# Kernel tuning notes

Measured on AMD Instinct MI355X. Metric: run time of the kernel, lower is better.

Reference implementation:

```python
import jax, jax.numpy as jnp
import numpy as np

B, D, C = 8192, 256, 128
MARGIN = 0.5
REPULSION_WEIGHT = 1.0
ALPHA = 0.5
BETA = 0.5
EPS = 1e-6  # F.pairwise_distance default eps, added to the difference vector


def make_centers(num_classes=C, embedding_dim=D):
    # center[k] is +/-1 one-hot along axis (k % embedding_dim)
    idx = np.arange(num_classes)
    centers = np.zeros((num_classes, embedding_dim), dtype=np.float32)
    centers[idx, idx % embedding_dim] = np.where(idx % 2 == 0, 1.0, -1.0)
    return jnp.asarray(centers)


def setup_inputs() -> dict:
    key = jax.random.key(0)
    k1, k2, k3 = jax.random.split(key, 3)
    features = jax.random.normal(k1, (B, D), dtype=jnp.float32)
    classification = jax.random.normal(k2, (B, C), dtype=jnp.float32)
    labels = jax.random.randint(k3, (B,), 0, C, dtype=jnp.int32)
    return {"features": features, "classification": classification, "labels": labels}


def _sculpted_loss(embeddings, labels, centers):
    b = embeddings.shape[0]
    # attractive: MSE to per-sample class center, mean over all elements
    center_targets = centers[labels]  # [B, D]
    attractive = jnp.mean((embeddings - center_targets) ** 2)

    # repulsive: for pairs i<j with different labels,
    # relu(margin - ||e_i - e_j + eps||_2)^2, summed then / (B(B-1)/2).
    sq_norm = jnp.sum(embeddings ** 2, axis=1)          # [B]
    row_sum = jnp.sum(embeddings, axis=1)               # [B]
    gram = embeddings @ embeddings.T                    # [B, B]
    sq = (sq_norm[:, None] + sq_norm[None, :] - 2.0 * gram
          + 2.0 * EPS * (row_sum[:, None] - row_sum[None, :])
          + embeddings.shape[1] * (EPS * EPS))
    dist = jnp.sqrt(jnp.maximum(sq, 1e-12))             # [B, B]

    iu = jnp.triu(jnp.ones((b, b), dtype=bool), k=1)    # i < j
    diff_label = labels[:, None] != labels[None, :]
    mask = iu & diff_label
    hinge = jnp.maximum(MARGIN - dist, 0.0)
    repulsive = jnp.sum(jnp.where(mask, hinge * hinge, 0.0))
    repulsive = repulsive / (b * (b - 1) / 2.0)

    return attractive + REPULSION_WEIGHT * repulsive


def reference(features, classification, labels):
    centers = make_centers()
    # cross entropy (mean over batch)
    logp = jax.nn.log_softmax(classification, axis=-1)
    ce = -jnp.mean(jnp.take_along_axis(logp, labels[:, None].astype(jnp.int32), axis=1)[:, 0])
    contrastive = _sculpted_loss(features, labels, centers)
    return BETA * contrastive + ALPHA * ce
```

## Files before the change

kernel.cpp:

```cpp
#include <hip/hip_runtime.h>
#include <stdint.h>

#define B_N   8192
#define D_DIM 256
#define C_CLS 128
#define EPSV  1e-6f
#define DEPS  (256.0f * EPSV * EPSV)
#define NT    64
#define NTRI  (NT * (NT + 1) / 2)
#define PLANE (B_N * 16)

typedef float f32x4 __attribute__((ext_vector_type(4)));
typedef long long llx2 __attribute__((ext_vector_type(2)));

__device__ __forceinline__ unsigned f2fp8(float v) {
    unsigned u = __float_as_uint(v);
    unsigned s = (u >> 24) & 0x80;
    unsigned a = u & 0x7fffffff;
    if (a > 0x43E00000u) a = 0x43E00000u;
    a += 0x7FFFF + ((a >> 20) & 1);
    int e = (int)(a >> 23) - 120;
    if (e <= 0) return s;
    return s | ((unsigned)e << 3) | ((a >> 20) & 7);
}


__global__ __launch_bounds__(256) void k_prep(
        const float* __restrict__ feat, const float* __restrict__ cls,
        const int* __restrict__ labels, unsigned char* __restrict__ e8,
        float* __restrict__ aR, float* __restrict__ bC,
        float* __restrict__ attrP, float* __restrict__ ceP) {
    int t = threadIdx.x, lane = t & 63, w = t >> 6;
    int row = blockIdx.x * 4 + w;
    int lab = labels[row];

    const float4* src = (const float4*)(feat + (size_t)row * D_DIM);
    float4 f = src[lane];
    unsigned pk = f2fp8(f.x) | (f2fp8(f.y) << 8) | (f2fp8(f.z) << 16) | (f2fp8(f.w) << 24);
    {
        int plane = ((lane >> 4) << 2) | ((lane >> 1) & 3);
        int off   = (((lane >> 3) & 1) << 3) | ((lane & 1) << 2);
        *(unsigned*)(e8 + (size_t)plane * PLANE + row * 16 + off) = pk;
    }

    float sq = f.x*f.x + f.y*f.y + f.z*f.z + f.w*f.w;
    float sm = f.x + f.y + f.z + f.w;
    float arr[4] = {f.x, f.y, f.z, f.w};
    float pick = ((lab >> 2) == lane) ? arr[lab & 3] : 0.f;

    const float2* csrc = (const float2*)(cls + (size_t)row * C_CLS);
    float2 c2 = csrc[lane];
    float mx = fmaxf(c2.x, c2.y);
    #pragma unroll
    for (int off = 32; off; off >>= 1) mx = fmaxf(mx, __shfl_xor(mx, off));
    float es = expf(c2.x - mx) + expf(c2.y - mx);
    float cpick = ((lab >> 1) == lane) ? ((lab & 1) ? c2.y : c2.x) : 0.f;

    #pragma unroll
    for (int off = 32; off; off >>= 1) {
        sq    += __shfl_xor(sq, off);
        sm    += __shfl_xor(sm, off);
        pick  += __shfl_xor(pick, off);
        es    += __shfl_xor(es, off);
        cpick += __shfl_xor(cpick, off);
    }
    __shared__ float wsumA[4], wsumC[4];
    if (lane == 0) {
        aR[row] = sq + 2.f * EPSV * sm;
        bC[row] = sq - 2.f * EPSV * sm + DEPS;
        float s = (lab & 1) ? -1.f : 1.f;
        wsumA[w] = sq - 2.f * s * pick + 1.f;
        wsumC[w] = -(cpick - mx - logf(es));
    }
    __syncthreads();
    if (t == 0) {
        attrP[blockIdx.x] = wsumA[0] + wsumA[1] + wsumA[2] + wsumA[3];
        ceP[blockIdx.x]   = wsumC[0] + wsumC[1] + wsumC[2] + wsumC[3];
    }
}

__global__ __launch_bounds__(256, 3) void k_gram(
        const unsigned char* __restrict__ e8, const float* __restrict__ aR,
        const float* __restrict__ bC, const int* __restrict__ labels,
        float* __restrict__ repP) {
    int t = threadIdx.x, lane = t & 63, w = t >> 6;

    int swz = (blockIdx.x & 7) * (NTRI / 8) + (blockIdx.x >> 3);

    int bid = swz, tm = 0;
    while (bid >= NT - tm) { bid -= NT - tm; tm++; }
    int tn = tm + bid;

    int l15 = lane & 15, quad = lane >> 4;
    int wr = w >> 1, wc = w & 1;
    int m0 = tm * 128 + wr * 64, n0 = tn * 128 + wc * 64;

    unsigned rowA[4], rowB[4];
    #pragma unroll
    for (int i = 0; i < 4; i++) {
        rowA[i] = (unsigned)(m0 + i * 16 + l15) * 16;
        rowB[i] = (unsigned)(n0 + i * 16 + l15) * 16;
    }

    f32x4 acc[4][4] = {};
    llx2 avA[4], bvA[4], avB[4], bvB[4];
    float am[16], bn[4];

    {
        const unsigned char* b0 = e8 + (size_t)quad * PLANE;
        #pragma unroll
        for (int mi = 0; mi < 4; mi++) avA[mi] = *(const llx2*)(b0 + rowA[mi]);
        #pragma unroll
        for (int ni = 0; ni < 4; ni++) bvA[ni] = *(const llx2*)(b0 + rowB[ni]);
    }

    #pragma unroll
    for (int tp = 0; tp < 4; tp++) {
        llx2* ca = (tp & 1) ? avB : avA;
        llx2* cb = (tp & 1) ? bvB : bvA;
        llx2* na = (tp & 1) ? avA : avB;
        llx2* nb = (tp & 1) ? bvA : bvB;
        if (tp < 3) {
            const unsigned char* bnx = e8 + (size_t)(4 * (tp + 1) + quad) * PLANE;
            #pragma unroll
            for (int mi = 0; mi < 4; mi++) na[mi] = *(const llx2*)(bnx + rowA[mi]);
            #pragma unroll
            for (int ni = 0; ni < 4; ni++) nb[ni] = *(const llx2*)(bnx + rowB[ni]);
        } else {
            #pragma unroll
            for (int ni = 0; ni < 4; ni++) bn[ni] = bC[n0 + ni * 16 + l15];
            #pragma unroll
            for (int mi = 0; mi < 4; mi++)
                #pragma unroll
                for (int r = 0; r < 4; r++)
                    am[mi * 4 + r] = aR[m0 + mi * 16 + quad * 4 + r];
        }
        __builtin_amdgcn_s_setprio(1);
        #pragma unroll
        for (int p = 0; p < 2; p++)
            #pragma unroll
            for (int mi = 0; mi < 4; mi++)
                #pragma unroll
                for (int ni = 0; ni < 4; ni++)
                    acc[mi][ni] = __builtin_amdgcn_mfma_f32_16x16x32_fp8_fp8(
                        ca[mi][p], cb[ni][p], acc[mi][ni], 0, 0, 0);
        __builtin_amdgcn_s_setprio(0);
    }

    float minv = 1e30f;
    #pragma unroll
    for (int mi = 0; mi < 4; mi++)
        #pragma unroll
        for (int ni = 0; ni < 4; ni++)
            #pragma unroll
            for (int r = 0; r < 4; r++)
                minv = fminf(minv, fmaf(-2.f, acc[mi][ni][r], am[mi * 4 + r] + bn[ni]));
    #pragma unroll
    for (int off = 32; off; off >>= 1) minv = fminf(minv, __shfl_xor(minv, off));

    float rep = 0.f;
    if (minv < 0.25f) {
        int ln[4];
        #pragma unroll
        for (int ni = 0; ni < 4; ni++) ln[ni] = labels[n0 + ni * 16 + l15];
        #pragma unroll
        for (int mi = 0; mi < 4; mi++) {
            #pragma unroll
            for (int r = 0; r < 4; r++) {
                int m = m0 + mi * 16 + quad * 4 + r;
                int lm = labels[m];
                #pragma unroll
                for (int ni = 0; ni < 4; ni++) {
                    int n = n0 + ni * 16 + l15;
                    float sq   = fmaf(-2.f, acc[mi][ni][r], am[mi * 4 + r] + bn[ni]);
                    float dist = sqrtf(fmaxf(sq, 1e-12f));
                    float h    = fmaxf(0.5f - dist, 0.f);
                    rep += (lm != ln[ni] && m < n) ? h * h : 0.f;
                }
            }
        }
        #pragma unroll
        for (int off = 32; off; off >>= 1) rep += __shfl_xor(rep, off);
    }
    if (lane == 0) repP[swz * 4 + w] = rep;
}

__global__ __launch_bounds__(256) void k_final(
        const float* __restrict__ P, float* __restrict__ out) {
    int t = threadIdx.x, lane = t & 63, w = t >> 6;
    const float4* P4 = (const float4*)P;
    float a = 0.f, c = 0.f, r = 0.f;
    for (int i = t; i < 512; i += 256) {
        float4 va = P4[i], vc = P4[512 + i];
        a += va.x + va.y + va.z + va.w;
        c += vc.x + vc.y + vc.z + vc.w;
    }
    for (int i = t; i < 2080; i += 256) {
        float4 vr = P4[1024 + i];
        r += vr.x + vr.y + vr.z + vr.w;
    }
    #pragma unroll
    for (int off = 32; off; off >>= 1) {
        a += __shfl_xor(a, off);
        c += __shfl_xor(c, off);
        r += __shfl_xor(r, off);
    }
    __shared__ float sa[4], sc[4], sr[4];
    if (lane == 0) { sa[w] = a; sc[w] = c; sr[w] = r; }
    __syncthreads();
    if (t == 0) {
        float attr = (sa[0] + sa[1] + sa[2] + sa[3]) / (float)((size_t)B_N * D_DIM);
        float ce   = (sc[0] + sc[1] + sc[2] + sc[3]) / (float)B_N;
        float rep  = (sr[0] + sr[1] + sr[2] + sr[3]) / ((float)B_N * (float)(B_N - 1) * 0.5f);
        out[0] = 0.5f * (attr + rep) + 0.5f * ce;
    }
}

extern "C" void kernel_launch(void* const* d_in, const int* in_sizes, int n_in,
                              void* d_out, int out_size, void* d_ws, size_t ws_size,
                              hipStream_t stream) {
    const float* feat   = (const float*)d_in[0];
    const float* cls    = (const float*)d_in[1];
    const int*   labels = (const int*)d_in[2];
    float* out = (float*)d_out;

    float*          P    = (float*)d_ws;
    unsigned char*  e8   = (unsigned char*)d_ws + 65536;
    float*          aR   = (float*)((char*)d_ws + 65536 + (size_t)B_N * D_DIM);
    float*          bC   = aR + B_N;

    k_prep <<<2048, 256, 0, stream>>>(feat, cls, labels, e8, aR, bC, P, P + 2048);
    k_gram <<<NTRI, 256, 0, stream>>>(e8, aR, bC, labels, P + 4096);
    k_final<<<1, 256, 0, stream>>>(P, out);
}
```

Baseline: 91.91 us.

## Prune gram tiles early using partial-dimension distance lower bound

The gram kernel now accumulates only the first 64 feature dimensions and computes a per-row norm and sum over that slice in the prep kernel. That gives a lower bound on each pairwise squared distance. If every pair in a tile has a partial squared distance at or above a safe threshold, the tile writes zero and exits without loading or multiplying the remaining three quarters of the data. The cost is extra prep outputs, the loss of double-buffered prefetching on the full path, and a data-dependent branch. Tiles near the diagonal or with close pairs still pay the full cost.

```diff
diff --git a/kernel.cpp b/kernel.cpp
--- a/kernel.cpp
+++ b/kernel.cpp
@@ -6,6 +6,7 @@
 #define C_CLS 128
 #define EPSV  1e-6f
 #define DEPS  (256.0f * EPSV * EPSV)
+#define D64EPS (64.0f * EPSV * EPSV)
 #define NT    64
 #define NTRI  (NT * (NT + 1) / 2)
 #define PLANE (B_N * 16)
@@ -29,6 +30,7 @@
         const float* __restrict__ feat, const float* __restrict__ cls,
         const int* __restrict__ labels, unsigned char* __restrict__ e8,
         float* __restrict__ aR, float* __restrict__ bC,
+        float* __restrict__ aR64, float* __restrict__ bC64,
         float* __restrict__ attrP, float* __restrict__ ceP) {
     int t = threadIdx.x, lane = t & 63, w = t >> 6;
     int row = blockIdx.x * 4 + w;
@@ -45,6 +47,8 @@
 
     float sq = f.x*f.x + f.y*f.y + f.z*f.z + f.w*f.w;
     float sm = f.x + f.y + f.z + f.w;
+    float sq64 = (lane < 16) ? sq : 0.f;
+    float sm64 = (lane < 16) ? sm : 0.f;
     float arr[4] = {f.x, f.y, f.z, f.w};
     float pick = ((lab >> 2) == lane) ? arr[lab & 3] : 0.f;
 
@@ -60,14 +64,18 @@
     for (int off = 32; off; off >>= 1) {
         sq    += __shfl_xor(sq, off);
         sm    += __shfl_xor(sm, off);
+        sq64  += __shfl_xor(sq64, off);
+        sm64  += __shfl_xor(sm64, off);
         pick  += __shfl_xor(pick, off);
         es    += __shfl_xor(es, off);
         cpick += __shfl_xor(cpick, off);
     }
     __shared__ float wsumA[4], wsumC[4];
     if (lane == 0) {
-        aR[row] = sq + 2.f * EPSV * sm;
-        bC[row] = sq - 2.f * EPSV * sm + DEPS;
+        aR[row]   = sq + 2.f * EPSV * sm;
+        bC[row]   = sq - 2.f * EPSV * sm + DEPS;
+        aR64[row] = sq64 + 2.f * EPSV * sm64;
+        bC64[row] = sq64 - 2.f * EPSV * sm64 + D64EPS;
         float s = (lab & 1) ? -1.f : 1.f;
         wsumA[w] = sq - 2.f * s * pick + 1.f;
         wsumC[w] = -(cpick - mx - logf(es));
@@ -81,7 +89,8 @@
 
 __global__ __launch_bounds__(256, 3) void k_gram(
         const unsigned char* __restrict__ e8, const float* __restrict__ aR,
-        const float* __restrict__ bC, const int* __restrict__ labels,
+        const float* __restrict__ bC, const float* __restrict__ aR64,
+        const float* __restrict__ bC64, const int* __restrict__ labels,
         float* __restrict__ repP) {
     int t = threadIdx.x, lane = t & 63, w = t >> 6;
 
@@ -103,38 +112,58 @@
     }
 
     f32x4 acc[4][4] = {};
-    llx2 avA[4], bvA[4], avB[4], bvB[4];
-    float am[16], bn[4];
+    llx2 av[4], bv[4];
 
     {
         const unsigned char* b0 = e8 + (size_t)quad * PLANE;
         #pragma unroll
-        for (int mi = 0; mi < 4; mi++) avA[mi] = *(const llx2*)(b0 + rowA[mi]);
-        #pragma unroll
-        for (int ni = 0; ni < 4; ni++) bvA[ni] = *(const llx2*)(b0 + rowB[ni]);
-    }
-
-    #pragma unroll
-    for (int tp = 0; tp < 4; tp++) {
-        llx2* ca = (tp & 1) ? avB : avA;
-        llx2* cb = (tp & 1) ? bvB : bvA;
-        llx2* na = (tp & 1) ? avA : avB;
-        llx2* nb = (tp & 1) ? bvA : bvB;
-        if (tp < 3) {
-            const unsigned char* bnx = e8 + (size_t)(4 * (tp + 1) + quad) * PLANE;
-            #pragma unroll
-            for (int mi = 0; mi < 4; mi++) na[mi] = *(const llx2*)(bnx + rowA[mi]);
-            #pragma unroll
-            for (int ni = 0; ni < 4; ni++) nb[ni] = *(const llx2*)(bnx + rowB[ni]);
-        } else {
-            #pragma unroll
-            for (int ni = 0; ni < 4; ni++) bn[ni] = bC[n0 + ni * 16 + l15];
-            #pragma unroll
-            for (int mi = 0; mi < 4; mi++)
-                #pragma unroll
-                for (int r = 0; r < 4; r++)
-                    am[mi * 4 + r] = aR[m0 + mi * 16 + quad * 4 + r];
-        }
+        for (int mi = 0; mi < 4; mi++) av[mi] = *(const llx2*)(b0 + rowA[mi]);
+        #pragma unroll
+        for (int ni = 0; ni < 4; ni++) bv[ni] = *(const llx2*)(b0 + rowB[ni]);
+    }
+    float am64[16], bn64[4];
+    #pragma unroll
+    for (int ni = 0; ni < 4; ni++) bn64[ni] = bC64[n0 + ni * 16 + l15];
+    #pragma unroll
+    for (int mi = 0; mi < 4; mi++)
+        #pragma unroll
+        for (int r = 0; r < 4; r++)
+            am64[mi * 4 + r] = aR64[m0 + mi * 16 + quad * 4 + r];
+
+    __builtin_amdgcn_s_setprio(1);
+    #pragma unroll
+    for (int p = 0; p < 2; p++)
+        #pragma unroll
+        for (int mi = 0; mi < 4; mi++)
+            #pragma unroll
+            for (int ni = 0; ni < 4; ni++)
+                acc[mi][ni] = __builtin_amdgcn_mfma_f32_16x16x32_fp8_fp8(
+                    av[mi][p], bv[ni][p], acc[mi][ni], 0, 0, 0);
+    __builtin_amdgcn_s_setprio(0);
+
+    float minv = 1e30f;
+    #pragma unroll
+    for (int mi = 0; mi < 4; mi++)
+        #pragma unroll
+        for (int ni = 0; ni < 4; ni++)
+            #pragma unroll
+            for (int r = 0; r < 4; r++)
+                minv = fminf(minv, fmaf(-2.f, acc[mi][ni][r], am64[mi * 4 + r] + bn64[ni]));
+    #pragma unroll
+    for (int off = 32; off; off >>= 1) minv = fminf(minv, __shfl_xor(minv, off));
+
+    if (minv >= 4.0f) {
+        if (lane == 0) repP[swz * 4 + w] = 0.f;
+        return;
+    }
+
+    #pragma unroll
+    for (int tp = 1; tp < 4; tp++) {
+        const unsigned char* bp = e8 + (size_t)(4 * tp + quad) * PLANE;
+        #pragma unroll
+        for (int mi = 0; mi < 4; mi++) av[mi] = *(const llx2*)(bp + rowA[mi]);
+        #pragma unroll
+        for (int ni = 0; ni < 4; ni++) bv[ni] = *(const llx2*)(bp + rowB[ni]);
         __builtin_amdgcn_s_setprio(1);
         #pragma unroll
         for (int p = 0; p < 2; p++)
@@ -143,11 +172,20 @@
                 #pragma unroll
                 for (int ni = 0; ni < 4; ni++)
                     acc[mi][ni] = __builtin_amdgcn_mfma_f32_16x16x32_fp8_fp8(
-                        ca[mi][p], cb[ni][p], acc[mi][ni], 0, 0, 0);
+                        av[mi][p], bv[ni][p], acc[mi][ni], 0, 0, 0);
         __builtin_amdgcn_s_setprio(0);
     }
 
-    float minv = 1e30f;
+    float am[16], bn[4];
+    #pragma unroll
+    for (int ni = 0; ni < 4; ni++) bn[ni] = bC[n0 + ni * 16 + l15];
+    #pragma unroll
+    for (int mi = 0; mi < 4; mi++)
+        #pragma unroll
+        for (int r = 0; r < 4; r++)
+            am[mi * 4 + r] = aR[m0 + mi * 16 + quad * 4 + r];
+
+    minv = 1e30f;
     #pragma unroll
     for (int mi = 0; mi < 4; mi++)
         #pragma unroll
@@ -228,8 +266,11 @@
     unsigned char*  e8   = (unsigned char*)d_ws + 65536;
     float*          aR   = (float*)((char*)d_ws + 65536 + (size_t)B_N * D_DIM);
     float*          bC   = aR + B_N;
-
-    k_prep <<<2048, 256, 0, stream>>>(feat, cls, labels, e8, aR, bC, P, P + 2048);
-    k_gram <<<NTRI, 256, 0, stream>>>(e8, aR, bC, labels, P + 4096);
+    float*          aR64 = bC + B_N;
+    float*          bC64 = aR64 + B_N;
+
+    k_prep <<<2048, 256, 0, stream>>>(feat, cls, labels, e8, aR, bC,
+                                      aR64, bC64, P, P + 2048);
+    k_gram <<<NTRI, 256, 0, stream>>>(e8, aR, bC, aR64, bC64, labels, P + 4096);
     k_final<<<1, 256, 0, stream>>>(P, out);
 }
```

Result: faster. 88.54 us (-3.7%).
